# Kernel optimization log

Measured on AMD Instinct MI355X. Metric: run time of the kernel, lower is better.

The kernel has to match this reference:

```python
import jax, jax.numpy as jnp
import numpy as np

B, T, H, C = 131072, 40, 40, 4  # batch, seq_len (=input_size), hidden_size, classes


def setup_inputs() -> dict:
    key = jax.random.key(0)
    ks = jax.random.split(key, 7)
    s = 1.0 / np.sqrt(H)  # PyTorch LSTM/Linear init scale
    x = jax.random.normal(ks[0], (B, T), dtype=jnp.float32)
    W_ih = jax.random.uniform(ks[1], (4 * H, 1), jnp.float32, -s, s)
    W_hh = jax.random.uniform(ks[2], (4 * H, H), jnp.float32, -s, s)
    b_ih = jax.random.uniform(ks[3], (4 * H,), jnp.float32, -s, s)
    b_hh = jax.random.uniform(ks[4], (4 * H,), jnp.float32, -s, s)
    W_fc = jax.random.uniform(ks[5], (C, H), jnp.float32, -s, s)
    b_fc = jax.random.uniform(ks[6], (C,), jnp.float32, -s, s)
    return {"x": x, "W_ih": W_ih, "W_hh": W_hh, "b_ih": b_ih, "b_hh": b_hh,
            "W_fc": W_fc, "b_fc": b_fc}


def _lstm_last_hidden(x, W_ih, W_hh, b_ih, b_hh):
    # x: [B, T] -> per-step input is scalar feature. PyTorch gate order: i, f, g, o.
    b = b_ih + b_hh  # [4H]
    w_in = W_ih[:, 0]  # [4H] since input_size == 1
    h0 = jnp.zeros((x.shape[0], H), dtype=x.dtype)
    c0 = jnp.zeros((x.shape[0], H), dtype=x.dtype)

    def step(carry, x_t):
        h, c = carry
        # gates: [B, 4H]
        g = x_t[:, None] * w_in[None, :] + h @ W_hh.T + b
        i, f, gg, o = jnp.split(g, 4, axis=1)
        i = jax.nn.sigmoid(i)
        f = jax.nn.sigmoid(f)
        gg = jnp.tanh(gg)
        o = jax.nn.sigmoid(o)
        c_new = f * c + i * gg
        h_new = o * jnp.tanh(c_new)
        return (h_new, c_new), None

    (h_T, _), _ = jax.lax.scan(step, (h0, c0), x.T)  # scan over time (T steps)
    return h_T  # [B, H]


def reference(x, W_ih, W_hh, b_ih, b_hh, W_fc, b_fc):
    # Dropout(0.2) is identity in eval mode.
    h_T = _lstm_last_hidden(x, W_ih, W_hh, b_ih, b_hh)
    logits = h_T @ W_fc.T + b_fc  # [B, C]
    return logits, jnp.argmax(logits, axis=1)
```

## Files before the change

kernel.cpp:

```cpp
#include <hip/hip_runtime.h>


#define B_    131072
#define T_    40
#define H_    40
#define C_    4
#define BLK   256
#define WPB   4
#define SPW   16
#define SPB   64
#define LROW  68
#define NT    10
#define LOG2E 1.44269504088896340736f

typedef __fp16   fp16x2 __attribute__((ext_vector_type(2)));
typedef _Float16 half2v __attribute__((ext_vector_type(2)));
typedef _Float16 half4v __attribute__((ext_vector_type(4)));
typedef _Float16 half8v __attribute__((ext_vector_type(8)));
typedef float    f32x2  __attribute__((ext_vector_type(2)));
typedef float    f32x4  __attribute__((ext_vector_type(4)));

__device__ __forceinline__ float fexp2f(float v){ return __builtin_amdgcn_exp2f(v); }
__device__ __forceinline__ float frcpf (float v){ return __builtin_amdgcn_rcpf(v); }

__device__ __forceinline__ f32x2 fexp2v(f32x2 v){ return (f32x2){fexp2f(v[0]), fexp2f(v[1])}; }
__device__ __forceinline__ f32x2 frcpv (f32x2 v){ return (f32x2){frcpf(v[0]),  frcpf(v[1])};  }

__device__ __forceinline__ f32x2 shflx8(f32x2 v){
    return (f32x2){ __shfl_xor(v[0], 8, 64), __shfl_xor(v[1], 8, 64) };
}

__device__ __forceinline__ half2v pkrtz(float a, float b) {
    fp16x2 r = __builtin_amdgcn_cvt_pkrtz(a, b);
    return __builtin_bit_cast(half2v, r);
}

__device__ __forceinline__ float himask(float v) {
    return __builtin_bit_cast(float, __builtin_bit_cast(unsigned int, v) & 0xFFFFE000u);
}

__device__ __forceinline__ void gates_act(const f32x4& ai, const f32x4& af,
                                          const f32x4& ag, const f32x4& ao,
                                          f32x2 (&cst)[2],
                                          float* wb, const int jt)
{
#pragma unroll
    for (int p = 0; p < 2; ++p) {
        const f32x2 yi = (f32x2){ai[2*p], ai[2*p+1]};
        const f32x2 yf = (f32x2){af[2*p], af[2*p+1]};
        const f32x2 yg = (f32x2){ag[2*p], ag[2*p+1]};
        const f32x2 yo = (f32x2){ao[2*p], ao[2*p+1]};
        const f32x2 ei = fexp2v(yi);
        const f32x2 ef = fexp2v(yf);
        const f32x2 Eg = fexp2v(yg);
        const f32x2 eo = fexp2v(yo);
        const f32x2 one = (f32x2){1.0f, 1.0f};
        const f32x2 u_ = one + ei;
        const f32x2 v_ = one + Eg;
        const f32x2 w_ = one + ef;
        const f32x2 p_ = u_ * v_;
        const f32x2 q_ = (Eg - one) * w_;
        const f32x2 num = cst[p] * p_ + q_;
        const f32x2 cn  = num * frcpv(p_ * w_);
        cst[p] = cn;
        const f32x2 Ec = fexp2v(cn * (f32x2){2.0f*LOG2E, 2.0f*LOG2E});
        const f32x2 hn = (Ec - one) * frcpv((one + eo) * (one + Ec));
        wb[(2*p)   * LROW + jt * 16] = hn[0];
        wb[(2*p+1) * LROW + jt * 16] = hn[1];
    }
}

__global__ __launch_bounds__(BLK, 2)
void lstm_mfma_kernel(const float* __restrict__ x,
                      const float* __restrict__ W_ih,
                      const float* __restrict__ W_hh,
                      const float* __restrict__ b_ih,
                      const float* __restrict__ b_hh,
                      const float* __restrict__ W_fc,
                      const float* __restrict__ b_fc,
                      float* __restrict__ out)
{
    __shared__ float lds[WPB * SPW * LROW];

    const int tid  = threadIdx.x;
    const int wv   = __builtin_amdgcn_readfirstlane(tid >> 6);
    const int lane = tid & 63;
    const int col  = lane & 15;
    const int quad = lane >> 4;
    const int sbase = blockIdx.x * SPB + wv * SPW;

    float* hbase = lds + wv * (SPW * LROW);

#pragma unroll
    for (int i = 0; i < (SPW * LROW) / 64; ++i)
        hbase[i * 64 + lane] = 0.0f;
    if (quad == 0) hbase[col * LROW + 41] = 1.0f;

    half8v Bh32[NT], Bl32[NT];
    half4v Bh16[NT], Bl16[NT];
#pragma unroll
    for (int tau = 0; tau < NT; ++tau) {
        int   r;
        float scale;
        if (tau < 8) {
            const int tt = tau >> 1;
            const int jt = tau & 1;
            r     = tt * H_ + jt * 16 + col;
            scale = (tt == 2) ? (2.0f * LOG2E) : (-LOG2E);
        } else if (tau == 8) {
            r     = (col < 8) ? (32 + col) : (H_ + 32 + (col - 8));
            scale = -LOG2E;
        } else {
            r     = (col < 8) ? (2 * H_ + 32 + col) : (3 * H_ + 32 + (col - 8));
            scale = (col < 8) ? (2.0f * LOG2E) : (-LOG2E);
        }

        {
            float4 w0 = *reinterpret_cast<const float4*>(W_hh + r * H_ + 8 * quad);
            float4 w1 = *reinterpret_cast<const float4*>(W_hh + r * H_ + 8 * quad + 4);
            float wa[8] = {w0.x, w0.y, w0.z, w0.w, w1.x, w1.y, w1.z, w1.w};
            half8v bh, bl;
#pragma unroll
            for (int j = 0; j < 8; ++j) {
                float w = wa[j] * scale;
                _Float16 hi = (_Float16)w;
                bh[j] = hi;
                bl[j] = (_Float16)(w - (float)hi);
            }
            Bh32[tau] = bh; Bl32[tau] = bl;
        }
        {
            float4 wv4;
            if (quad == 0)      wv4 = *reinterpret_cast<const float4*>(W_hh + r * H_ + 32);
            else if (quad == 1) wv4 = *reinterpret_cast<const float4*>(W_hh + r * H_ + 36);
            else if (quad == 2) wv4 = make_float4(W_ih[r], b_ih[r] + b_hh[r], 0.0f, 0.0f);
            else                wv4 = make_float4(0.0f, 0.0f, 0.0f, 0.0f);
            float wa[4] = {wv4.x, wv4.y, wv4.z, wv4.w};
            half4v bh, bl;
#pragma unroll
            for (int j = 0; j < 4; ++j) {
                float w = wa[j] * scale;
                _Float16 hi = (_Float16)w;
                bh[j] = hi;
                bl[j] = (_Float16)(w - (float)hi);
            }
            Bh16[tau] = bh; Bl16[tau] = bl;
        }
    }

    f32x2 cst2[3][2];
#pragma unroll
    for (int jt = 0; jt < 3; ++jt) {
        cst2[jt][0] = (f32x2){0.f, 0.f};
        cst2[jt][1] = (f32x2){0.f, 0.f};
    }

    const f32x4 zc = (f32x4){0.f, 0.f, 0.f, 0.f};

    const float* myrow = hbase + col * LROW;
    const float* a32p  = myrow + 8 * quad;
    const float* a16p  = myrow + 32 + 4 * quad;
    float* xslot  = hbase + col * LROW + 40;
    float* wbase  = hbase + 4 * quad * LROW + col;
    float* wbase2 = wbase + ((col >= 8) ? 8 : 0) + 32;

    const float* xrow = x + (long)(sbase + col) * T_;
    float xv = xrow[0];
    if (quad == 0) *xslot = xv;

    f32x4 hv0 = *reinterpret_cast<const f32x4*>(a32p);
    f32x4 hv1 = *reinterpret_cast<const f32x4*>(a32p + 4);
    f32x4 hv2 = *reinterpret_cast<const f32x4*>(a16p);

#pragma unroll 1
    for (int t = 0; t < T_; ++t) {
        const int tn = (t + 1 < T_) ? (t + 1) : (T_ - 1);
        const float xnext = xrow[tn];

        half8v ah32, al32; half4v ah16, al16;
        {
            f32x4 hi0, hi1, hi2;
#pragma unroll
            for (int j = 0; j < 4; ++j) {
                hi0[j] = himask(hv0[j]);
                hi1[j] = himask(hv1[j]);
                hi2[j] = himask(hv2[j]);
            }
            f32x4 lo0 = hv0 - hi0;
            f32x4 lo1 = hv1 - hi1;
            f32x4 lo2 = hv2 - hi2;

            half2v h00 = pkrtz(hi0[0], hi0[1]);
            half2v h01 = pkrtz(hi0[2], hi0[3]);
            half2v h10 = pkrtz(hi1[0], hi1[1]);
            half2v h11 = pkrtz(hi1[2], hi1[3]);
            half2v l00 = pkrtz(lo0[0], lo0[1]);
            half2v l01 = pkrtz(lo0[2], lo0[3]);
            half2v l10 = pkrtz(lo1[0], lo1[1]);
            half2v l11 = pkrtz(lo1[2], lo1[3]);
            half2v h20 = pkrtz(hi2[0], hi2[1]);
            half2v h21 = pkrtz(hi2[2], hi2[3]);
            half2v l20 = pkrtz(lo2[0], lo2[1]);
            half2v l21 = pkrtz(lo2[2], lo2[3]);

            half4v a0 = __builtin_shufflevector(h00, h01, 0, 1, 2, 3);
            half4v a1 = __builtin_shufflevector(h10, h11, 0, 1, 2, 3);
            ah32 = __builtin_shufflevector(a0, a1, 0, 1, 2, 3, 4, 5, 6, 7);
            half4v b0 = __builtin_shufflevector(l00, l01, 0, 1, 2, 3);
            half4v b1 = __builtin_shufflevector(l10, l11, 0, 1, 2, 3);
            al32 = __builtin_shufflevector(b0, b1, 0, 1, 2, 3, 4, 5, 6, 7);
            ah16 = __builtin_shufflevector(h20, h21, 0, 1, 2, 3);
            al16 = __builtin_shufflevector(l20, l21, 0, 1, 2, 3);
        }

#define DOT48(tau, dst)                                                          \
        {                                                                        \
            f32x4 a_ = __builtin_amdgcn_mfma_f32_16x16x32_f16(ah32, Bh32[tau], zc, 0, 0, 0); \
            a_ = __builtin_amdgcn_mfma_f32_16x16x32_f16(al32, Bh32[tau], a_, 0, 0, 0); \
            a_ = __builtin_amdgcn_mfma_f32_16x16x32_f16(ah32, Bl32[tau], a_, 0, 0, 0); \
            a_ = __builtin_amdgcn_mfma_f32_16x16x16f16(ah16, Bh16[tau], a_, 0, 0, 0); \
            a_ = __builtin_amdgcn_mfma_f32_16x16x16f16(al16, Bh16[tau], a_, 0, 0, 0); \
            a_ = __builtin_amdgcn_mfma_f32_16x16x16f16(ah16, Bl16[tau], a_, 0, 0, 0); \
            dst = a_;                                                            \
        }

#pragma unroll
        for (int jt = 0; jt < 2; ++jt) {
            f32x4 ai, af, ag, ao;
            DOT48(0 + jt, ai)
            DOT48(2 + jt, af)
            DOT48(4 + jt, ag)
            DOT48(6 + jt, ao)
            gates_act(ai, af, ag, ao, cst2[jt], wbase, jt);
        }

        hv0 = *reinterpret_cast<const f32x4*>(a32p);
        hv1 = *reinterpret_cast<const f32x4*>(a32p + 4);

        {
            f32x4 aif, ago;
            DOT48(8, aif)
            DOT48(9, ago)
#pragma unroll
            for (int p = 0; p < 2; ++p) {
                const f32x2 y1 = (f32x2){aif[2*p], aif[2*p+1]};
                const f32x2 y2 = (f32x2){ago[2*p], ago[2*p+1]};
                const f32x2 e1 = fexp2v(y1);
                const f32x2 e2 = fexp2v(y2);
                const f32x2 one = (f32x2){1.0f, 1.0f};
                const f32x2 s1 = one + e1;
                const f32x2 s2 = one + e2;
                const f32x2 w_ = shflx8(s1);
                const f32x2 oe = shflx8(s2);
                const f32x2 p_ = s1 * s2;
                const f32x2 q_ = (e2 - one) * w_;
                const f32x2 num = cst2[2][p] * p_ + q_;
                const f32x2 cn  = num * frcpv(p_ * w_);
                cst2[2][p] = cn;
                const f32x2 Ec = fexp2v(cn * (f32x2){2.0f*LOG2E, 2.0f*LOG2E});
                const f32x2 hn = (Ec - one) * frcpv(oe * (one + Ec));
                wbase2[(2*p)   * LROW] = hn[0];
                wbase2[(2*p+1) * LROW] = hn[1];
            }
        }

        if (quad == 0) *xslot = xnext;
        hv2 = *reinterpret_cast<const f32x4*>(a16p);
#undef DOT48
    }

    {
        float acc = b_fc[quad];
#pragma unroll
        for (int jj = 0; jj < 10; ++jj) {
            f32x4 hv = *reinterpret_cast<const f32x4*>(myrow + 4 * jj);
            float4 wv4 = *reinterpret_cast<const float4*>(W_fc + quad * H_ + 4 * jj);
            acc = fmaf(hv[0], wv4.x, acc);
            acc = fmaf(hv[1], wv4.y, acc);
            acc = fmaf(hv[2], wv4.z, acc);
            acc = fmaf(hv[3], wv4.w, acc);
        }
        out[(long)(sbase + col) * C_ + quad] = acc;
        hbase[col * LROW + 56 + quad] = acc;
    }
    if (quad == 0) {
        f32x4 lg = *reinterpret_cast<const f32x4*>(hbase + col * LROW + 56);
        int am = 0;
        float best = lg[0];
        if (lg[1] > best) { best = lg[1]; am = 1; }
        if (lg[2] > best) { best = lg[2]; am = 2; }
        if (lg[3] > best) { best = lg[3]; am = 3; }
        out[(long)B_ * C_ + sbase + col] = (float)am;
    }
}

extern "C" void kernel_launch(void* const* d_in, const int* in_sizes, int n_in,
                              void* d_out, int out_size, void* d_ws, size_t ws_size,
                              hipStream_t stream) {
    const float* x    = (const float*)d_in[0];
    const float* W_ih = (const float*)d_in[1];
    const float* W_hh = (const float*)d_in[2];
    const float* b_ih = (const float*)d_in[3];
    const float* b_hh = (const float*)d_in[4];
    const float* W_fc = (const float*)d_in[5];
    const float* b_fc = (const float*)d_in[6];
    float* out = (float*)d_out;

    dim3 block(BLK);
    dim3 grid(B_ / SPB);
    hipLaunchKernelGGL(lstm_mfma_kernel, grid, block, 0, stream,
                       x, W_ih, W_hh, b_ih, b_hh, W_fc, b_fc, out);
}
```

Measured before the change: 381.1 us.

## Interleave two independent 16-sequence recurrences per wave to hide MFMA latency

```diff
diff --git a/kernel.cpp b/kernel.cpp
--- a/kernel.cpp
+++ b/kernel.cpp
@@ -7,8 +7,8 @@
 #define C_    4
 #define BLK   256
 #define WPB   4
-#define SPW   16
-#define SPB   64
+#define SPW   32
+#define SPB   128
 #define LROW  68
 #define NT    10
 #define LOG2E 1.44269504088896340736f
@@ -37,6 +37,44 @@
 
 __device__ __forceinline__ float himask(float v) {
     return __builtin_bit_cast(float, __builtin_bit_cast(unsigned int, v) & 0xFFFFE000u);
+}
+
+__device__ __forceinline__ void mk_frags(const f32x4 hv0, const f32x4 hv1, const f32x4 hv2,
+                                         half8v& ah32, half8v& al32,
+                                         half4v& ah16, half4v& al16)
+{
+    f32x4 hi0, hi1, hi2;
+#pragma unroll
+    for (int j = 0; j < 4; ++j) {
+        hi0[j] = himask(hv0[j]);
+        hi1[j] = himask(hv1[j]);
+        hi2[j] = himask(hv2[j]);
+    }
+    f32x4 lo0 = hv0 - hi0;
+    f32x4 lo1 = hv1 - hi1;
+    f32x4 lo2 = hv2 - hi2;
+
+    half2v h00 = pkrtz(hi0[0], hi0[1]);
+    half2v h01 = pkrtz(hi0[2], hi0[3]);
+    half2v h10 = pkrtz(hi1[0], hi1[1]);
+    half2v h11 = pkrtz(hi1[2], hi1[3]);
+    half2v l00 = pkrtz(lo0[0], lo0[1]);
+    half2v l01 = pkrtz(lo0[2], lo0[3]);
+    half2v l10 = pkrtz(lo1[0], lo1[1]);
+    half2v l11 = pkrtz(lo1[2], lo1[3]);
+    half2v h20 = pkrtz(hi2[0], hi2[1]);
+    half2v h21 = pkrtz(hi2[2], hi2[3]);
+    half2v l20 = pkrtz(lo2[0], lo2[1]);
+    half2v l21 = pkrtz(lo2[2], lo2[3]);
+
+    half4v a0 = __builtin_shufflevector(h00, h01, 0, 1, 2, 3);
+    half4v a1 = __builtin_shufflevector(h10, h11, 0, 1, 2, 3);
+    ah32 = __builtin_shufflevector(a0, a1, 0, 1, 2, 3, 4, 5, 6, 7);
+    half4v b0 = __builtin_shufflevector(l00, l01, 0, 1, 2, 3);
+    half4v b1 = __builtin_shufflevector(l10, l11, 0, 1, 2, 3);
+    al32 = __builtin_shufflevector(b0, b1, 0, 1, 2, 3, 4, 5, 6, 7);
+    ah16 = __builtin_shufflevector(h20, h21, 0, 1, 2, 3);
+    al16 = __builtin_shufflevector(l20, l21, 0, 1, 2, 3);
 }
 
 __device__ __forceinline__ void gates_act(const f32x4& ai, const f32x4& af,
@@ -70,6 +108,32 @@
     }
 }
 
+__device__ __forceinline__ void act_jt2(const f32x4& aif, const f32x4& ago,
+                                        f32x2 (&cst)[2], float* wb2)
+{
+#pragma unroll
+    for (int p = 0; p < 2; ++p) {
+        const f32x2 y1 = (f32x2){aif[2*p], aif[2*p+1]};
+        const f32x2 y2 = (f32x2){ago[2*p], ago[2*p+1]};
+        const f32x2 e1 = fexp2v(y1);
+        const f32x2 e2 = fexp2v(y2);
+        const f32x2 one = (f32x2){1.0f, 1.0f};
+        const f32x2 s1 = one + e1;
+        const f32x2 s2 = one + e2;
+        const f32x2 w_ = shflx8(s1);
+        const f32x2 oe = shflx8(s2);
+        const f32x2 p_ = s1 * s2;
+        const f32x2 q_ = (e2 - one) * w_;
+        const f32x2 num = cst[p] * p_ + q_;
+        const f32x2 cn  = num * frcpv(p_ * w_);
+        cst[p] = cn;
+        const f32x2 Ec = fexp2v(cn * (f32x2){2.0f*LOG2E, 2.0f*LOG2E});
+        const f32x2 hn = (Ec - one) * frcpv(oe * (one + Ec));
+        wb2[(2*p)   * LROW] = hn[0];
+        wb2[(2*p+1) * LROW] = hn[1];
+    }
+}
+
 __global__ __launch_bounds__(BLK, 2)
 void lstm_mfma_kernel(const float* __restrict__ x,
                       const float* __restrict__ W_ih,
@@ -89,12 +153,13 @@
     const int quad = lane >> 4;
     const int sbase = blockIdx.x * SPB + wv * SPW;
 
-    float* hbase = lds + wv * (SPW * LROW);
+    float* baseA = lds + wv * (SPW * LROW);
+    float* baseB = baseA + 16 * LROW;
 
 #pragma unroll
     for (int i = 0; i < (SPW * LROW) / 64; ++i)
-        hbase[i * 64 + lane] = 0.0f;
-    if (quad == 0) hbase[col * LROW + 41] = 1.0f;
+        baseA[i * 64 + lane] = 0.0f;
+    if (quad < 2) baseA[quad * 16 * LROW + col * LROW + 41] = 1.0f;
 
     half8v Bh32[NT], Bl32[NT];
     half4v Bh16[NT], Bl16[NT];
@@ -148,128 +213,115 @@
         }
     }
 
-    f32x2 cst2[3][2];
+    f32x2 cstA[3][2], cstB[3][2];
 #pragma unroll
     for (int jt = 0; jt < 3; ++jt) {
-        cst2[jt][0] = (f32x2){0.f, 0.f};
-        cst2[jt][1] = (f32x2){0.f, 0.f};
+        cstA[jt][0] = (f32x2){0.f, 0.f}; cstA[jt][1] = (f32x2){0.f, 0.f};
+        cstB[jt][0] = (f32x2){0.f, 0.f}; cstB[jt][1] = (f32x2){0.f, 0.f};
     }
 
     const f32x4 zc = (f32x4){0.f, 0.f, 0.f, 0.f};
 
-    const float* myrow = hbase + col * LROW;
-    const float* a32p  = myrow + 8 * quad;
-    const float* a16p  = myrow + 32 + 4 * quad;
-    float* xslot  = hbase + col * LROW + 40;
-    float* wbase  = hbase + 4 * quad * LROW + col;
-    float* wbase2 = wbase + ((col >= 8) ? 8 : 0) + 32;
-
-    const float* xrow = x + (long)(sbase + col) * T_;
-    float xv = xrow[0];
-    if (quad == 0) *xslot = xv;
-
-    f32x4 hv0 = *reinterpret_cast<const f32x4*>(a32p);
-    f32x4 hv1 = *reinterpret_cast<const f32x4*>(a32p + 4);
-    f32x4 hv2 = *reinterpret_cast<const f32x4*>(a16p);
+    const float* a32pA = baseA + col * LROW + 8 * quad;
+    const float* a16pA = baseA + col * LROW + 32 + 4 * quad;
+    const float* a32pB = baseB + col * LROW + 8 * quad;
+    const float* a16pB = baseB + col * LROW + 32 + 4 * quad;
+    float* xslotA = baseA + col * LROW + 40;
+    float* xslotB = baseB + col * LROW + 40;
+    float* wbA  = baseA + 4 * quad * LROW + col;
+    float* wbB  = baseB + 4 * quad * LROW + col;
+    float* wb2A = wbA + ((col >= 8) ? 8 : 0) + 32;
+    float* wb2B = wbB + ((col >= 8) ? 8 : 0) + 32;
+
+    const float* xrowA = x + (long)(sbase + col) * T_;
+    const float* xrowB = x + (long)(sbase + 16 + col) * T_;
+    float xvA = xrowA[0];
+    float xvB = xrowB[0];
+    if (quad == 0) *xslotA = xvA;
+    if (quad == 1) *xslotB = xvB;
+
+    f32x4 hvA0 = *reinterpret_cast<const f32x4*>(a32pA);
+    f32x4 hvA1 = *reinterpret_cast<const f32x4*>(a32pA + 4);
+    f32x4 hvA2 = *reinterpret_cast<const f32x4*>(a16pA);
+    f32x4 hvB0 = *reinterpret_cast<const f32x4*>(a32pB);
+    f32x4 hvB1 = *reinterpret_cast<const f32x4*>(a32pB + 4);
+    f32x4 hvB2 = *reinterpret_cast<const f32x4*>(a16pB);
+
+#define DOT48(AH32, AL32, AH16, AL16, tau, dst)                                  \
+    {                                                                            \
+        f32x4 a_ = __builtin_amdgcn_mfma_f32_16x16x32_f16(AH32, Bh32[tau], zc, 0, 0, 0); \
+        a_ = __builtin_amdgcn_mfma_f32_16x16x32_f16(AL32, Bh32[tau], a_, 0, 0, 0); \
+        a_ = __builtin_amdgcn_mfma_f32_16x16x32_f16(AH32, Bl32[tau], a_, 0, 0, 0); \
+        a_ = __builtin_amdgcn_mfma_f32_16x16x16f16(AH16, Bh16[tau], a_, 0, 0, 0); \
+        a_ = __builtin_amdgcn_mfma_f32_16x16x16f16(AL16, Bh16[tau], a_, 0, 0, 0); \
+        a_ = __builtin_amdgcn_mfma_f32_16x16x16f16(AH16, Bl16[tau], a_, 0, 0, 0); \
+        dst = a_;                                                                \
+    }
 
 #pragma unroll 1
     for (int t = 0; t < T_; ++t) {
         const int tn = (t + 1 < T_) ? (t + 1) : (T_ - 1);
-        const float xnext = xrow[tn];
-
-        half8v ah32, al32; half4v ah16, al16;
-        {
-            f32x4 hi0, hi1, hi2;
-#pragma unroll
-            for (int j = 0; j < 4; ++j) {
-                hi0[j] = himask(hv0[j]);
-                hi1[j] = himask(hv1[j]);
-                hi2[j] = himask(hv2[j]);
-            }
-            f32x4 lo0 = hv0 - hi0;
-            f32x4 lo1 = hv1 - hi1;
-            f32x4 lo2 = hv2 - hi2;
-
-            half2v h00 = pkrtz(hi0[0], hi0[1]);
-            half2v h01 = pkrtz(hi0[2], hi0[3]);
-            half2v h10 = pkrtz(hi1[0], hi1[1]);
-            half2v h11 = pkrtz(hi1[2], hi1[3]);
-            half2v l00 = pkrtz(lo0[0], lo0[1]);
-            half2v l01 = pkrtz(lo0[2], lo0[3]);
-            half2v l10 = pkrtz(lo1[0], lo1[1]);
-            half2v l11 = pkrtz(lo1[2], lo1[3]);
-            half2v h20 = pkrtz(hi2[0], hi2[1]);
-            half2v h21 = pkrtz(hi2[2], hi2[3]);
-            half2v l20 = pkrtz(lo2[0], lo2[1]);
-            half2v l21 = pkrtz(lo2[2], lo2[3]);
-
-            half4v a0 = __builtin_shufflevector(h00, h01, 0, 1, 2, 3);
-            half4v a1 = __builtin_shufflevector(h10, h11, 0, 1, 2, 3);
-            ah32 = __builtin_shufflevector(a0, a1, 0, 1, 2, 3, 4, 5, 6, 7);
-            half4v b0 = __builtin_shufflevector(l00, l01, 0, 1, 2, 3);
-            half4v b1 = __builtin_shufflevector(l10, l11, 0, 1, 2, 3);
-            al32 = __builtin_shufflevector(b0, b1, 0, 1, 2, 3, 4, 5, 6, 7);
-            ah16 = __builtin_shufflevector(h20, h21, 0, 1, 2, 3);
-            al16 = __builtin_shufflevector(l20, l21, 0, 1, 2, 3);
-        }
-
-#define DOT48(tau, dst)                                                          \
-        {                                                                        \
-            f32x4 a_ = __builtin_amdgcn_mfma_f32_16x16x32_f16(ah32, Bh32[tau], zc, 0, 0, 0); \
-            a_ = __builtin_amdgcn_mfma_f32_16x16x32_f16(al32, Bh32[tau], a_, 0, 0, 0); \
-            a_ = __builtin_amdgcn_mfma_f32_16x16x32_f16(ah32, Bl32[tau], a_, 0, 0, 0); \
-            a_ = __builtin_amdgcn_mfma_f32_16x16x16f16(ah16, Bh16[tau], a_, 0, 0, 0); \
-            a_ = __builtin_amdgcn_mfma_f32_16x16x16f16(al16, Bh16[tau], a_, 0, 0, 0); \
-            a_ = __builtin_amdgcn_mfma_f32_16x16x16f16(ah16, Bl16[tau], a_, 0, 0, 0); \
-            dst = a_;                                                            \
-        }
-
-#pragma unroll
-        for (int jt = 0; jt < 2; ++jt) {
-            f32x4 ai, af, ag, ao;
-            DOT48(0 + jt, ai)
-            DOT48(2 + jt, af)
-            DOT48(4 + jt, ag)
-            DOT48(6 + jt, ao)
-            gates_act(ai, af, ag, ao, cst2[jt], wbase, jt);
-        }
-
-        hv0 = *reinterpret_cast<const f32x4*>(a32p);
-        hv1 = *reinterpret_cast<const f32x4*>(a32p + 4);
-
-        {
-            f32x4 aif, ago;
-            DOT48(8, aif)
-            DOT48(9, ago)
-#pragma unroll
-            for (int p = 0; p < 2; ++p) {
-                const f32x2 y1 = (f32x2){aif[2*p], aif[2*p+1]};
-                const f32x2 y2 = (f32x2){ago[2*p], ago[2*p+1]};
-                const f32x2 e1 = fexp2v(y1);
-                const f32x2 e2 = fexp2v(y2);
-                const f32x2 one = (f32x2){1.0f, 1.0f};
-                const f32x2 s1 = one + e1;
-                const f32x2 s2 = one + e2;
-                const f32x2 w_ = shflx8(s1);
-                const f32x2 oe = shflx8(s2);
-                const f32x2 p_ = s1 * s2;
-                const f32x2 q_ = (e2 - one) * w_;
-                const f32x2 num = cst2[2][p] * p_ + q_;
-                const f32x2 cn  = num * frcpv(p_ * w_);
-                cst2[2][p] = cn;
-                const f32x2 Ec = fexp2v(cn * (f32x2){2.0f*LOG2E, 2.0f*LOG2E});
-                const f32x2 hn = (Ec - one) * frcpv(oe * (one + Ec));
-                wbase2[(2*p)   * LROW] = hn[0];
-                wbase2[(2*p+1) * LROW] = hn[1];
-            }
-        }
-
-        if (quad == 0) *xslot = xnext;
-        hv2 = *reinterpret_cast<const f32x4*>(a16p);
+        const float xnA = xrowA[tn];
+        const float xnB = xrowB[tn];
+
+        half8v aA32h, aA32l; half4v aA16h, aA16l;
+        half8v aB32h, aB32l; half4v aB16h, aB16l;
+        mk_frags(hvA0, hvA1, hvA2, aA32h, aA32l, aA16h, aA16l);
+        mk_frags(hvB0, hvB1, hvB2, aB32h, aB32l, aB16h, aB16l);
+
+        {
+            f32x4 Ai, Af, Ag, Ao, Bi, Bf, Bg, Bo;
+            DOT48(aA32h, aA32l, aA16h, aA16l, 0, Ai)
+            DOT48(aA32h, aA32l, aA16h, aA16l, 2, Af)
+            DOT48(aA32h, aA32l, aA16h, aA16l, 4, Ag)
+            DOT48(aA32h, aA32l, aA16h, aA16l, 6, Ao)
+            DOT48(aB32h, aB32l, aB16h, aB16l, 0, Bi)
+            DOT48(aB32h, aB32l, aB16h, aB16l, 2, Bf)
+            DOT48(aB32h, aB32l, aB16h, aB16l, 4, Bg)
+            DOT48(aB32h, aB32l, aB16h, aB16l, 6, Bo)
+            gates_act(Ai, Af, Ag, Ao, cstA[0], wbA, 0);
+            gates_act(Bi, Bf, Bg, Bo, cstB[0], wbB, 0);
+        }
+
+        {
+            f32x4 Ai, Af, Ag, Ao, Bi, Bf, Bg, Bo;
+            DOT48(aA32h, aA32l, aA16h, aA16l, 1, Ai)
+            DOT48(aA32h, aA32l, aA16h, aA16l, 3, Af)
+            DOT48(aA32h, aA32l, aA16h, aA16l, 5, Ag)
+            DOT48(aA32h, aA32l, aA16h, aA16l, 7, Ao)
+            DOT48(aB32h, aB32l, aB16h, aB16l, 1, Bi)
+            DOT48(aB32h, aB32l, aB16h, aB16l, 3, Bf)
+            DOT48(aB32h, aB32l, aB16h, aB16l, 5, Bg)
+            DOT48(aB32h, aB32l, aB16h, aB16l, 7, Bo)
+            gates_act(Ai, Af, Ag, Ao, cstA[1], wbA, 1);
+            hvA0 = *reinterpret_cast<const f32x4*>(a32pA);
+            hvA1 = *reinterpret_cast<const f32x4*>(a32pA + 4);
+            gates_act(Bi, Bf, Bg, Bo, cstB[1], wbB, 1);
+            hvB0 = *reinterpret_cast<const f32x4*>(a32pB);
+            hvB1 = *reinterpret_cast<const f32x4*>(a32pB + 4);
+        }
+
+        {
+            f32x4 Aif, Ago, Bif, Bgo;
+            DOT48(aA32h, aA32l, aA16h, aA16l, 8, Aif)
+            DOT48(aA32h, aA32l, aA16h, aA16l, 9, Ago)
+            DOT48(aB32h, aB32l, aB16h, aB16l, 8, Bif)
+            DOT48(aB32h, aB32l, aB16h, aB16l, 9, Bgo)
+            act_jt2(Aif, Ago, cstA[2], wb2A);
+            act_jt2(Bif, Bgo, cstB[2], wb2B);
+        }
+
+        if (quad == 0) *xslotA = xnA;
+        if (quad == 1) *xslotB = xnB;
+        hvA2 = *reinterpret_cast<const f32x4*>(a16pA);
+        hvB2 = *reinterpret_cast<const f32x4*>(a16pB);
+    }
 #undef DOT48
-    }
-
-    {
+
+#pragma unroll
+    for (int c = 0; c < 2; ++c) {
+        const float* myrow = (c == 0 ? baseA : baseB) + col * LROW;
+        float* hb = (c == 0 ? baseA : baseB);
         float acc = b_fc[quad];
 #pragma unroll
         for (int jj = 0; jj < 10; ++jj) {
@@ -280,17 +332,21 @@
             acc = fmaf(hv[2], wv4.z, acc);
             acc = fmaf(hv[3], wv4.w, acc);
         }
-        out[(long)(sbase + col) * C_ + quad] = acc;
-        hbase[col * LROW + 56 + quad] = acc;
+        out[(long)(sbase + c * 16 + col) * C_ + quad] = acc;
+        hb[col * LROW + 56 + quad] = acc;
     }
     if (quad == 0) {
-        f32x4 lg = *reinterpret_cast<const f32x4*>(hbase + col * LROW + 56);
-        int am = 0;
-        float best = lg[0];
-        if (lg[1] > best) { best = lg[1]; am = 1; }
-        if (lg[2] > best) { best = lg[2]; am = 2; }
-        if (lg[3] > best) { best = lg[3]; am = 3; }
-        out[(long)B_ * C_ + sbase + col] = (float)am;
+#pragma unroll
+        for (int c = 0; c < 2; ++c) {
+            const float* hb = (c == 0 ? baseA : baseB);
+            f32x4 lg = *reinterpret_cast<const f32x4*>(hb + col * LROW + 56);
+            int am = 0;
+            float best = lg[0];
+            if (lg[1] > best) { best = lg[1]; am = 1; }
+            if (lg[2] > best) { best = lg[2]; am = 2; }
+            if (lg[3] > best) { best = lg[3]; am = 3; }
+            out[(long)B_ * C_ + sbase + c * 16 + col] = (float)am;
+        }
     }
 }
 
```

After: 383.7 us. About the same (+0.7%).
